# Performance work log

Measured on AMD Instinct MI355X. Metric: run time of the kernel, lower is better.

Reference implementation:

```python
import jax, jax.numpy as jnp
import numpy as np

N = 100000   # nodes
E = 1600000  # edges
IN, H, C = 128, 128, 40


def setup_inputs() -> dict:
    key = jax.random.key(0)
    ks = jax.random.split(key, 8)
    feat = jax.random.normal(ks[0], (N, IN), jnp.float32)
    src = jax.random.randint(ks[1], (E,), 0, N, jnp.int32)
    dst = jax.random.randint(ks[2], (E,), 0, N, jnp.int32)
    # Glorot-ish init like dgl GraphConv.reset_parameters
    W0 = jax.random.normal(ks[3], (IN, H), jnp.float32) * (1.0 / np.sqrt(IN))
    W1 = jax.random.normal(ks[4], (H, H), jnp.float32) * (1.0 / np.sqrt(H))
    W2 = jax.random.normal(ks[5], (H, C), jnp.float32) * (1.0 / np.sqrt(H))
    b0 = jnp.zeros((H,), jnp.float32)
    b1 = jnp.zeros((H,), jnp.float32)
    b2 = jnp.zeros((C,), jnp.float32)
    return {"feat": feat, "src": src, "dst": dst,
            "W0": W0, "b0": b0, "W1": W1, "b1": b1, "W2": W2, "b2": b2}


def _graph_conv(h, src, dst, W, b):
    # dgl GraphConv with norm='both': D_out^{-1/2} pre-scale, sum-aggregate,
    # D_in^{-1/2} post-scale; degrees clamped to min 1. Weight applied before
    # aggregation (in_feats >= out_feats path) -- math is identical either way.
    ones = jnp.ones((src.shape[0],), h.dtype)
    deg_out = jnp.maximum(jax.ops.segment_sum(ones, src, num_segments=N), 1.0)
    deg_in = jnp.maximum(jax.ops.segment_sum(ones, dst, num_segments=N), 1.0)
    h = h * (deg_out ** -0.5)[:, None]
    h = h @ W                                   # [N, out]
    agg = jax.ops.segment_sum(h[src], dst, num_segments=N)  # gather+scatter
    return agg * (deg_in ** -0.5)[:, None] + b


def reference(feat, src, dst, W0, b0, W1, b1, W2, b2):
    h = jax.nn.relu(_graph_conv(feat, src, dst, W0, b0))  # dropout p=0 -> identity
    h = jax.nn.relu(_graph_conv(h, src, dst, W1, b1))
    return _graph_conv(h, src, dst, W2, b2)
```

## Files before the change

kernel.cpp:

```cpp
#include <hip/hip_runtime.h>

#define NN 100000
#define EE 1600000
#define ELLW 64
#define GEMMN ((NN + 31) / 32)
#define BQ ((EE / 4 + 511) / 512)
#define GRID_BG (BQ * 5)

#define NBKT 196
#define BSH 9
#define CAPD 10240
#define CAPS 10240

typedef int iv4 __attribute__((ext_vector_type(4)));

__device__ __forceinline__ unsigned int pack_bf2(float a, float b) {
    unsigned int ua = __float_as_uint(a);
    ua += 0x7FFFu + ((ua >> 16) & 1u);
    unsigned int ub = __float_as_uint(b);
    ub += 0x7FFFu + ((ub >> 16) & 1u);
    return (ua >> 16) | (ub & 0xFFFF0000u);
}

__device__ __forceinline__ void gemm128_body(const float* __restrict__ X,
                                             const float* __restrict__ W, unsigned int* __restrict__ Y,
                                             int row0, int tid, float* Xs) {
    const float4* X4 = (const float4*)X;
#pragma unroll
    for (int idx = tid; idx < 1024; idx += 256) {
        int r = idx & 31, c4 = idx >> 5;
        int row = row0 + r;
        float4 v = X4[(size_t)row * 32 + c4];
        Xs[(c4 * 4 + 0) * 32 + r] = v.x;
        Xs[(c4 * 4 + 1) * 32 + r] = v.y;
        Xs[(c4 * 4 + 2) * 32 + r] = v.z;
        Xs[(c4 * 4 + 3) * 32 + r] = v.w;
    }
    __syncthreads();
    int cg = tid & 31;
    int rg = tid >> 5;
    float a[4][4];
#pragma unroll
    for (int r = 0; r < 4; ++r)
#pragma unroll
        for (int c = 0; c < 4; ++c) a[r][c] = 0.f;
    const float4* W4 = (const float4*)W;
#pragma unroll 4
    for (int k = 0; k < 128; ++k) {
        float4 xv = *(const float4*)&Xs[k * 32 + rg * 4];
        float4 wv = W4[k * 32 + cg];
        float xr[4] = {xv.x, xv.y, xv.z, xv.w};
        float wc[4] = {wv.x, wv.y, wv.z, wv.w};
#pragma unroll
        for (int r = 0; r < 4; ++r)
#pragma unroll
            for (int c = 0; c < 4; ++c) a[r][c] = fmaf(xr[r], wc[c], a[r][c]);
    }
    int rbase = row0 + rg * 4;
    uint2* Y2 = (uint2*)Y;
#pragma unroll
    for (int r = 0; r < 4; ++r) {
        Y2[(size_t)(rbase + r) * 32 + cg] =
            make_uint2(pack_bf2(a[r][0], a[r][1]), pack_bf2(a[r][2], a[r][3]));
    }
}

__global__ __launch_bounds__(256) void k_buildA_gemm0(const int* __restrict__ src, const int* __restrict__ dst,
                                                      int* __restrict__ curD, int* __restrict__ curS,
                                                      unsigned int* __restrict__ stagD,
                                                      unsigned short* __restrict__ stagS,
                                                      const float* __restrict__ X, const float* __restrict__ W,
                                                      unsigned int* __restrict__ Y) {
    __shared__ float Xs[128 * 32];
    int tid = threadIdx.x;
    int q = blockIdx.x / 5, rem = blockIdx.x % 5;
    if (rem) {
        int g = q * 4 + (rem - 1);
        if (g < GEMMN) gemm128_body(X, W, Y, g * 32, tid, Xs);
        return;
    }
    int* sh = (int*)Xs;
    for (int i = tid; i < 1536; i += 256) sh[i] = 0;
    __syncthreads();

    const iv4* s4p = (const iv4*)src;
    const iv4* d4p = (const iv4*)dst;
    const int n4 = EE / 4;
    iv4 sv[2], dv[2];
    int have[2];
#pragma unroll
    for (int h = 0; h < 2; ++h) {
        int i4 = q * 512 + h * 256 + tid;
        have[h] = (i4 < n4);
        if (have[h]) {
            sv[h] = __builtin_nontemporal_load(&s4p[i4]);
            dv[h] = __builtin_nontemporal_load(&d4p[i4]);
        }
    }
#pragma unroll
    for (int h = 0; h < 2; ++h) {
        if (have[h]) {
            int ss[4] = {sv[h].x, sv[h].y, sv[h].z, sv[h].w};
            int dd[4] = {dv[h].x, dv[h].y, dv[h].z, dv[h].w};
#pragma unroll
            for (int k = 0; k < 4; ++k) {
                atomicAdd(&sh[dd[k] >> BSH], 1);
                atomicAdd(&sh[256 + (ss[k] >> BSH)], 1);
            }
        }
    }
    __syncthreads();
    if (tid < NBKT) {
        int hd = sh[tid];
        sh[512 + tid] = hd ? atomicAdd(&curD[tid], hd) : 0;
        int hs = sh[256 + tid];
        sh[768 + tid] = hs ? atomicAdd(&curS[tid], hs) : 0;
    }
    __syncthreads();
#pragma unroll
    for (int h = 0; h < 2; ++h) {
        if (have[h]) {
            int ss[4] = {sv[h].x, sv[h].y, sv[h].z, sv[h].w};
            int dd[4] = {dv[h].x, dv[h].y, dv[h].z, dv[h].w};
#pragma unroll
            for (int k = 0; k < 4; ++k) {
                int bd = dd[k] >> BSH;
                int od = atomicAdd(&sh[1024 + bd], 1);
                stagD[(size_t)bd * CAPD + sh[512 + bd] + od] =
                    ((unsigned int)ss[k] << BSH) | (unsigned int)(dd[k] & 511);
                int bs = ss[k] >> BSH;
                int os = atomicAdd(&sh[1280 + bs], 1);
                stagS[(size_t)bs * CAPS + sh[768 + bs] + os] = (unsigned short)(ss[k] & 511);
            }
        }
    }
}

__global__ __launch_bounds__(256) void k_buildB(const int* __restrict__ curD, const int* __restrict__ curS,
                                                const unsigned int* __restrict__ stagD,
                                                const unsigned short* __restrict__ stagS,
                                                int* __restrict__ din, int* __restrict__ dout,
                                                int* __restrict__ ell) {
    __shared__ int cl[512];
    int tid = threadIdx.x;
    int b = blockIdx.x;
    for (int i = tid; i < 512; i += 256) cl[i] = 0;
    __syncthreads();
    if (b < NBKT) {
        int n0 = b << BSH;
        int cnt = min(curD[b], CAPD);
        const unsigned int* sg = stagD + (size_t)b * CAPD;
        for (int i = tid; i < cnt; i += 256) {
            unsigned int v = sg[i];
            int dlow = (int)(v & 511u);
            int s = (int)(v >> BSH);
            int p = atomicAdd(&cl[dlow], 1);
            if (p < ELLW) ell[(size_t)(n0 + dlow) * ELLW + p] = s;
        }
        __syncthreads();
        for (int i = tid; i < 512; i += 256) {
            int node = n0 + i;
            if (node < NN) din[node] = cl[i];
        }
    } else {
        int bs = b - NBKT;
        int n0 = bs << BSH;
        int cnt = min(curS[bs], CAPS);
        const unsigned short* sg = stagS + (size_t)bs * CAPS;
        for (int i = tid; i < cnt; i += 256) {
            atomicAdd(&cl[sg[i]], 1);
        }
        __syncthreads();
        for (int i = tid; i < 512; i += 256) {
            int node = n0 + i;
            if (node < NN) dout[node] = cl[i];
        }
    }
}

#define GG_BATCH(CL, SC, JB, CNT, SO) do {                                         \
    int cc_[8]; float mk_[8]; uint2 t_[8];                                         \
    _Pragma("unroll")                                                              \
    for (int k = 0; k < 8; ++k) {                                                  \
        int slot = (JB) + k;                                                       \
        int srcl = (hl << 5) | (slot & 31);                                        \
        cc_[k] = __shfl((CL), srcl);                                               \
        float sw = (SO) ? __shfl((SC), srcl) : 1.f;                                \
        mk_[k] = (slot < (CNT)) ? sw : 0.f;                                        \
    }                                                                              \
    _Pragma("unroll")                                                              \
    for (int k = 0; k < 8; ++k) {                                                  \
        t_[k] = make_uint2(0u, 0u);                                                \
        if ((JB) + k < (CNT)) t_[k] = h2v[(size_t)cc_[k] * 32 + ln];               \
    }                                                                              \
    _Pragma("unroll")                                                              \
    for (int k = 0; k < 8; ++k) {                                                  \
        a0 = fmaf(mk_[k], __uint_as_float(t_[k].x << 16), a0);                     \
        a1 = fmaf(mk_[k], __uint_as_float(t_[k].x & 0xFFFF0000u), a1);             \
        a2 = fmaf(mk_[k], __uint_as_float(t_[k].y << 16), a2);                     \
        a3 = fmaf(mk_[k], __uint_as_float(t_[k].y & 0xFFFF0000u), a3);             \
    }                                                                              \
} while (0)

__global__ __launch_bounds__(256) void k_gathergemm128(const unsigned int* __restrict__ h,
                                                       const int* __restrict__ din, const int* __restrict__ dout,
                                                       const int* __restrict__ ell,
                                                       const float* __restrict__ bias,
                                                       const float* __restrict__ W,
                                                       unsigned int* __restrict__ Y, int so_mode) {
    __shared__ float Xs[128 * 36];
    int tid = threadIdx.x;
    int wv = tid >> 6, lane = tid & 63;
    int hl = lane >> 5, ln = lane & 31;
    int row0 = blockIdx.x * 32;
    int nb = row0 + wv * 8 + hl;
    int dvh[4], dvo[4], cl0[4], cl1[4];
    float sc0[4], sc1[4];
#pragma unroll
    for (int it = 0; it < 4; ++it) {
        int v = nb + it * 2;
        dvh[it] = din[v];
        dvo[it] = dout[v];
        cl0[it] = ell[(size_t)v * ELLW + ln];
        cl1[it] = ell[(size_t)v * ELLW + 32 + ln];
    }
#pragma unroll
    for (int it = 0; it < 4; ++it) {
        int cnt = min(dvh[it], ELLW);
        int d0 = 1, d1 = 1;
        if (so_mode && ln < cnt) d0 = dout[cl0[it]];
        if (so_mode && ln + 32 < cnt) d1 = dout[cl1[it]];
        sc0[it] = rsqrtf((float)max(1, d0));
        sc1[it] = rsqrtf((float)max(1, d1));
    }
    float4 bb = ((const float4*)bias)[ln];
    const uint2* h2v = (const uint2*)h;
#pragma unroll
    for (int it = 0; it < 4; ++it) {
        int r = wv * 8 + it * 2 + hl;
        int cnt = min(dvh[it], ELLW);
        float a0 = 0.f, a1 = 0.f, a2 = 0.f, a3 = 0.f;
        for (int jb = 0; jb < 32; jb += 8) {
            if (!__any(jb < cnt)) break;
            GG_BATCH(cl0[it], sc0[it], jb, cnt, so_mode);
        }
        if (__any(cnt > 32)) {
            for (int jb = 32; jb < 64; jb += 8) {
                if (!__any(jb < cnt)) break;
                GG_BATCH(cl1[it], sc1[it], jb, cnt, so_mode);
            }
        }
        float si = rsqrtf((float)max(1, dvh[it]));
        float so = rsqrtf((float)max(1, dvo[it]));
        Xs[(4 * ln + 0) * 36 + r] = fmaxf(a0 * si + bb.x, 0.f) * so;
        Xs[(4 * ln + 1) * 36 + r] = fmaxf(a1 * si + bb.y, 0.f) * so;
        Xs[(4 * ln + 2) * 36 + r] = fmaxf(a2 * si + bb.z, 0.f) * so;
        Xs[(4 * ln + 3) * 36 + r] = fmaxf(a3 * si + bb.w, 0.f) * so;
    }
    __syncthreads();
    int cg = tid & 31, rg = tid >> 5;
    float a[4][4];
#pragma unroll
    for (int r = 0; r < 4; ++r)
#pragma unroll
        for (int c = 0; c < 4; ++c) a[r][c] = 0.f;
    const float4* W4 = (const float4*)W;
#pragma unroll 4
    for (int k = 0; k < 128; ++k) {
        float4 xv = *(const float4*)&Xs[k * 36 + rg * 4];
        float4 wv4 = W4[k * 32 + cg];
        float xr[4] = {xv.x, xv.y, xv.z, xv.w};
        float wc[4] = {wv4.x, wv4.y, wv4.z, wv4.w};
#pragma unroll
        for (int r = 0; r < 4; ++r)
#pragma unroll
            for (int c = 0; c < 4; ++c) a[r][c] = fmaf(xr[r], wc[c], a[r][c]);
    }
    int rbase = row0 + rg * 4;
    uint2* Y2 = (uint2*)Y;
#pragma unroll
    for (int r = 0; r < 4; ++r) {
        Y2[(size_t)(rbase + r) * 32 + cg] =
            make_uint2(pack_bf2(a[r][0], a[r][1]), pack_bf2(a[r][2], a[r][3]));
    }
}

__global__ __launch_bounds__(256) void k_gathergemm40(const unsigned int* __restrict__ h,
                                                      const int* __restrict__ din, const int* __restrict__ dout,
                                                      const int* __restrict__ ell,
                                                      const float* __restrict__ bias,
                                                      const float* __restrict__ W,
                                                      unsigned int* __restrict__ Y) {
    __shared__ float Xs[128 * 36];
    __shared__ float Os[32 * 40];
    int tid = threadIdx.x;
    int wv = tid >> 6, lane = tid & 63;
    int hl = lane >> 5, ln = lane & 31;
    int row0 = blockIdx.x * 32;
    int nb = row0 + wv * 8 + hl;
    int dvh[4], dvo[4], cl0[4], cl1[4];
#pragma unroll
    for (int it = 0; it < 4; ++it) {
        int v = nb + it * 2;
        dvh[it] = din[v];
        dvo[it] = dout[v];
        cl0[it] = ell[(size_t)v * ELLW + ln];
        cl1[it] = ell[(size_t)v * ELLW + 32 + ln];
    }
    float4 bb = ((const float4*)bias)[ln];
    const uint2* h2v = (const uint2*)h;
#pragma unroll
    for (int it = 0; it < 4; ++it) {
        int r = wv * 8 + it * 2 + hl;
        int cnt = min(dvh[it], ELLW);
        float a0 = 0.f, a1 = 0.f, a2 = 0.f, a3 = 0.f;
        float dummy = 0.f;
        for (int jb = 0; jb < 32; jb += 8) {
            if (!__any(jb < cnt)) break;
            GG_BATCH(cl0[it], dummy, jb, cnt, 0);
        }
        if (__any(cnt > 32)) {
            for (int jb = 32; jb < 64; jb += 8) {
                if (!__any(jb < cnt)) break;
                GG_BATCH(cl1[it], dummy, jb, cnt, 0);
            }
        }
        float si = rsqrtf((float)max(1, dvh[it]));
        float so = rsqrtf((float)max(1, dvo[it]));
        Xs[(4 * ln + 0) * 36 + r] = fmaxf(a0 * si + bb.x, 0.f) * so;
        Xs[(4 * ln + 1) * 36 + r] = fmaxf(a1 * si + bb.y, 0.f) * so;
        Xs[(4 * ln + 2) * 36 + r] = fmaxf(a2 * si + bb.z, 0.f) * so;
        Xs[(4 * ln + 3) * 36 + r] = fmaxf(a3 * si + bb.w, 0.f) * so;
    }
    __syncthreads();
    int rg = tid >> 3;
    int cg = tid & 7;
    float a[5] = {0.f, 0.f, 0.f, 0.f, 0.f};
    for (int k = 0; k < 128; ++k) {
        float x = Xs[k * 36 + rg];
#pragma unroll
        for (int c = 0; c < 5; ++c) a[c] = fmaf(x, W[k * 40 + cg * 5 + c], a[c]);
    }
#pragma unroll
    for (int c = 0; c < 5; ++c) Os[rg * 40 + cg * 5 + c] = a[c];
    __syncthreads();
    for (int i = tid; i < 640; i += 256) {
        int row = i / 20, pj = i % 20;
        Y[(size_t)(row0 + row) * 32 + pj] = pack_bf2(Os[row * 40 + 2 * pj], Os[row * 40 + 2 * pj + 1]);
    }
}

__global__ __launch_bounds__(256) void k_gather40(const unsigned int* __restrict__ h, const int* __restrict__ din,
                                                  const int* __restrict__ ell,
                                                  const float* __restrict__ b, float* __restrict__ out, int n) {
    int tid = threadIdx.x;
    int wv = tid >> 6, lane = tid & 63;
    int hl = lane >> 5, ln = lane & 31;
    int v = blockIdx.x * 8 + wv * 2 + hl;
    int dv = din[v];
    int cnt = min(dv, ELLW);
    int cl0 = ell[(size_t)v * ELLW + ln];
    int cl1 = ell[(size_t)v * ELLW + 32 + ln];
    float s0 = 0.f, s1 = 0.f;
    for (int half = 0; half < 2; ++half) {
        int clh = half ? cl1 : cl0;
        int jb0 = half * 32;
        if (half && !__any(cnt > 32)) break;
        for (int jb = jb0; jb < jb0 + 32; jb += 8) {
            if (!__any(jb < cnt)) break;
            int cc_[8]; float mk_[8]; unsigned int t_[8];
#pragma unroll
            for (int k = 0; k < 8; ++k) {
                int slot = jb + k;
                int srcl = (hl << 5) | (slot & 31);
                cc_[k] = __shfl(clh, srcl);
                mk_[k] = (slot < cnt) ? 1.f : 0.f;
            }
#pragma unroll
            for (int k = 0; k < 8; ++k) {
                t_[k] = 0u;
                if (jb + k < cnt) t_[k] = h[(size_t)cc_[k] * 32 + ln];
            }
#pragma unroll
            for (int k = 0; k < 8; ++k) {
                s0 = fmaf(mk_[k], __uint_as_float(t_[k] << 16), s0);
                s1 = fmaf(mk_[k], __uint_as_float(t_[k] & 0xFFFF0000u), s1);
            }
        }
    }
    if (ln < 20) {
        float si = rsqrtf((float)max(1, dv));
        float2 bb = ((const float2*)b)[ln];
        ((float2*)out)[(size_t)v * 20 + ln] = make_float2(s0 * si + bb.x, s1 * si + bb.y);
    }
}

extern "C" void kernel_launch(void* const* d_in, const int* in_sizes, int n_in,
                              void* d_out, int out_size, void* d_ws, size_t ws_size,
                              hipStream_t stream) {
    const float* feat = (const float*)d_in[0];
    const int*   src  = (const int*)d_in[1];
    const int*   dst  = (const int*)d_in[2];
    const float* W0   = (const float*)d_in[3];
    const float* b0   = (const float*)d_in[4];
    const float* W1   = (const float*)d_in[5];
    const float* b1   = (const float*)d_in[6];
    const float* W2   = (const float*)d_in[7];
    const float* b2   = (const float*)d_in[8];
    float* out = (float*)d_out;

    char* w = (char*)d_ws;
    int*   din       = (int*)w;    w += (size_t)NN * 4;
    int*   dout      = (int*)w;    w += (size_t)NN * 4;
    int*   curD      = (int*)w;    w += 256 * 4;
    int*   curS      = (int*)w;    w += 256 * 4;
    int*   ell       = (int*)w;    w += (size_t)NN * ELLW * 4;
    unsigned int*   stagD = (unsigned int*)w;   w += (size_t)NBKT * CAPD * 4;
    unsigned short* stagS = (unsigned short*)w; w += (size_t)NBKT * CAPS * 2;
    unsigned int* h2 = (unsigned int*)w; w += (size_t)NN * 128 * 2;
    unsigned int* h2b = (unsigned int*)w; w += (size_t)NN * 128 * 2;
    unsigned int* h40 = (unsigned int*)w; w += (size_t)NN * 32 * 4;

    (void)hipMemsetAsync(d_ws, 0, (size_t)NN * 8 + 2048, stream);

    k_buildA_gemm0<<<GRID_BG, 256, 0, stream>>>(src, dst, curD, curS, stagD, stagS, feat, W0, h2);
    k_buildB<<<NBKT * 2, 256, 0, stream>>>(curD, curS, stagD, stagS, din, dout, ell);
    k_gathergemm128<<<GEMMN, 256, 0, stream>>>(h2, din, dout, ell, b0, W1, h2b, 1);
    k_gathergemm40<<<GEMMN, 256, 0, stream>>>(h2b, din, dout, ell, b1, W2, h40);
    k_gather40<<<NN / 8, 256, 0, stream>>>(h40, din, ell, b2, out, NN);
}
```

Baseline: 480.0 us.

## Split fused gather+GEMM into half-width gather kernels and separate GEMM kernels

```diff
diff --git a/kernel.cpp b/kernel.cpp
--- a/kernel.cpp
+++ b/kernel.cpp
@@ -6,6 +6,7 @@
 #define GEMMN ((NN + 31) / 32)
 #define BQ ((EE / 4 + 511) / 512)
 #define GRID_BG (BQ * 5)
+#define GHGRID 6256
 
 #define NBKT 196
 #define BSH 9
@@ -178,41 +179,42 @@
     }
 }
 
-#define GG_BATCH(CL, SC, JB, CNT, SO) do {                                         \
-    int cc_[8]; float mk_[8]; uint2 t_[8];                                         \
+#define GH_BATCH(CL, SC, JB, CNT) do {                                             \
+    int cc_[8]; float mk_[8]; unsigned int t_[8];                                  \
     _Pragma("unroll")                                                              \
     for (int k = 0; k < 8; ++k) {                                                  \
         int slot = (JB) + k;                                                       \
         int srcl = (hl << 5) | (slot & 31);                                        \
         cc_[k] = __shfl((CL), srcl);                                               \
-        float sw = (SO) ? __shfl((SC), srcl) : 1.f;                                \
+        float sw = so_mode ? __shfl((SC), srcl) : 1.f;                             \
         mk_[k] = (slot < (CNT)) ? sw : 0.f;                                        \
     }                                                                              \
     _Pragma("unroll")                                                              \
     for (int k = 0; k < 8; ++k) {                                                  \
-        t_[k] = make_uint2(0u, 0u);                                                \
-        if ((JB) + k < (CNT)) t_[k] = h2v[(size_t)cc_[k] * 32 + ln];               \
+        t_[k] = 0u;                                                                \
+        if ((JB) + k < (CNT)) t_[k] = hh[(size_t)cc_[k] * 64 + ln];                \
     }                                                                              \
     _Pragma("unroll")                                                              \
     for (int k = 0; k < 8; ++k) {                                                  \
-        a0 = fmaf(mk_[k], __uint_as_float(t_[k].x << 16), a0);                     \
-        a1 = fmaf(mk_[k], __uint_as_float(t_[k].x & 0xFFFF0000u), a1);             \
-        a2 = fmaf(mk_[k], __uint_as_float(t_[k].y << 16), a2);                     \
-        a3 = fmaf(mk_[k], __uint_as_float(t_[k].y & 0xFFFF0000u), a3);             \
+        a0 = fmaf(mk_[k], __uint_as_float(t_[k] << 16), a0);                       \
+        a1 = fmaf(mk_[k], __uint_as_float(t_[k] & 0xFFFF0000u), a1);               \
     }                                                                              \
 } while (0)
 
-__global__ __launch_bounds__(256) void k_gathergemm128(const unsigned int* __restrict__ h,
-                                                       const int* __restrict__ din, const int* __restrict__ dout,
-                                                       const int* __restrict__ ell,
-                                                       const float* __restrict__ bias,
-                                                       const float* __restrict__ W,
-                                                       unsigned int* __restrict__ Y, int so_mode) {
-    __shared__ float Xs[128 * 36];
+__global__ __launch_bounds__(256) void k_gathalf(const unsigned int* __restrict__ h,
+                                                 const int* __restrict__ din, const int* __restrict__ dout,
+                                                 const int* __restrict__ ell,
+                                                 const float* __restrict__ bias,
+                                                 float* __restrict__ Xb, int so_mode) {
     int tid = threadIdx.x;
     int wv = tid >> 6, lane = tid & 63;
     int hl = lane >> 5, ln = lane & 31;
-    int row0 = blockIdx.x * 32;
+    int bid = blockIdx.x;
+    int xg = bid & 7;
+    int half = xg >> 2;
+    int t = (bid >> 3) * 4 + (xg & 3);
+    if (t >= GEMMN) return;
+    int row0 = t * 32;
     int nb = row0 + wv * 8 + hl;
     int dvh[4], dvo[4], cl0[4], cl1[4];
     float sc0[4], sc1[4];
@@ -233,111 +235,59 @@
         sc0[it] = rsqrtf((float)max(1, d0));
         sc1[it] = rsqrtf((float)max(1, d1));
     }
-    float4 bb = ((const float4*)bias)[ln];
-    const uint2* h2v = (const uint2*)h;
+    float2 bb = ((const float2*)bias)[32 * half + ln];
+    const unsigned int* hh = h + 32 * half;
 #pragma unroll
     for (int it = 0; it < 4; ++it) {
-        int r = wv * 8 + it * 2 + hl;
+        int v = nb + it * 2;
         int cnt = min(dvh[it], ELLW);
-        float a0 = 0.f, a1 = 0.f, a2 = 0.f, a3 = 0.f;
+        float a0 = 0.f, a1 = 0.f;
         for (int jb = 0; jb < 32; jb += 8) {
             if (!__any(jb < cnt)) break;
-            GG_BATCH(cl0[it], sc0[it], jb, cnt, so_mode);
+            GH_BATCH(cl0[it], sc0[it], jb, cnt);
         }
         if (__any(cnt > 32)) {
             for (int jb = 32; jb < 64; jb += 8) {
                 if (!__any(jb < cnt)) break;
-                GG_BATCH(cl1[it], sc1[it], jb, cnt, so_mode);
+                GH_BATCH(cl1[it], sc1[it], jb, cnt);
             }
         }
         float si = rsqrtf((float)max(1, dvh[it]));
         float so = rsqrtf((float)max(1, dvo[it]));
-        Xs[(4 * ln + 0) * 36 + r] = fmaxf(a0 * si + bb.x, 0.f) * so;
-        Xs[(4 * ln + 1) * 36 + r] = fmaxf(a1 * si + bb.y, 0.f) * so;
-        Xs[(4 * ln + 2) * 36 + r] = fmaxf(a2 * si + bb.z, 0.f) * so;
-        Xs[(4 * ln + 3) * 36 + r] = fmaxf(a3 * si + bb.w, 0.f) * so;
-    }
-    __syncthreads();
-    int cg = tid & 31, rg = tid >> 5;
-    float a[4][4];
-#pragma unroll
-    for (int r = 0; r < 4; ++r)
-#pragma unroll
-        for (int c = 0; c < 4; ++c) a[r][c] = 0.f;
-    const float4* W4 = (const float4*)W;
-#pragma unroll 4
-    for (int k = 0; k < 128; ++k) {
-        float4 xv = *(const float4*)&Xs[k * 36 + rg * 4];
-        float4 wv4 = W4[k * 32 + cg];
-        float xr[4] = {xv.x, xv.y, xv.z, xv.w};
-        float wc[4] = {wv4.x, wv4.y, wv4.z, wv4.w};
-#pragma unroll
-        for (int r = 0; r < 4; ++r)
-#pragma unroll
-            for (int c = 0; c < 4; ++c) a[r][c] = fmaf(xr[r], wc[c], a[r][c]);
-    }
-    int rbase = row0 + rg * 4;
-    uint2* Y2 = (uint2*)Y;
-#pragma unroll
-    for (int r = 0; r < 4; ++r) {
-        Y2[(size_t)(rbase + r) * 32 + cg] =
-            make_uint2(pack_bf2(a[r][0], a[r][1]), pack_bf2(a[r][2], a[r][3]));
-    }
-}
-
-__global__ __launch_bounds__(256) void k_gathergemm40(const unsigned int* __restrict__ h,
-                                                      const int* __restrict__ din, const int* __restrict__ dout,
-                                                      const int* __restrict__ ell,
-                                                      const float* __restrict__ bias,
-                                                      const float* __restrict__ W,
-                                                      unsigned int* __restrict__ Y) {
-    __shared__ float Xs[128 * 36];
+        float x0 = fmaxf(a0 * si + bb.x, 0.f) * so;
+        float x1 = fmaxf(a1 * si + bb.y, 0.f) * so;
+        ((float2*)Xb)[(size_t)v * 64 + 32 * half + ln] = make_float2(x0, x1);
+    }
+}
+
+__global__ __launch_bounds__(256) void k_gemm128(const float* __restrict__ X, const float* __restrict__ W,
+                                                 unsigned int* __restrict__ Y) {
+    __shared__ float Xs[128 * 32];
+    gemm128_body(X, W, Y, blockIdx.x * 32, threadIdx.x, Xs);
+}
+
+__global__ __launch_bounds__(256) void k_gemm40(const float* __restrict__ X, const float* __restrict__ W,
+                                                unsigned int* __restrict__ Y) {
+    __shared__ float Xs[128 * 32];
     __shared__ float Os[32 * 40];
     int tid = threadIdx.x;
-    int wv = tid >> 6, lane = tid & 63;
-    int hl = lane >> 5, ln = lane & 31;
     int row0 = blockIdx.x * 32;
-    int nb = row0 + wv * 8 + hl;
-    int dvh[4], dvo[4], cl0[4], cl1[4];
-#pragma unroll
-    for (int it = 0; it < 4; ++it) {
-        int v = nb + it * 2;
-        dvh[it] = din[v];
-        dvo[it] = dout[v];
-        cl0[it] = ell[(size_t)v * ELLW + ln];
-        cl1[it] = ell[(size_t)v * ELLW + 32 + ln];
-    }
-    float4 bb = ((const float4*)bias)[ln];
-    const uint2* h2v = (const uint2*)h;
-#pragma unroll
-    for (int it = 0; it < 4; ++it) {
-        int r = wv * 8 + it * 2 + hl;
-        int cnt = min(dvh[it], ELLW);
-        float a0 = 0.f, a1 = 0.f, a2 = 0.f, a3 = 0.f;
-        float dummy = 0.f;
-        for (int jb = 0; jb < 32; jb += 8) {
-            if (!__any(jb < cnt)) break;
-            GG_BATCH(cl0[it], dummy, jb, cnt, 0);
-        }
-        if (__any(cnt > 32)) {
-            for (int jb = 32; jb < 64; jb += 8) {
-                if (!__any(jb < cnt)) break;
-                GG_BATCH(cl1[it], dummy, jb, cnt, 0);
-            }
-        }
-        float si = rsqrtf((float)max(1, dvh[it]));
-        float so = rsqrtf((float)max(1, dvo[it]));
-        Xs[(4 * ln + 0) * 36 + r] = fmaxf(a0 * si + bb.x, 0.f) * so;
-        Xs[(4 * ln + 1) * 36 + r] = fmaxf(a1 * si + bb.y, 0.f) * so;
-        Xs[(4 * ln + 2) * 36 + r] = fmaxf(a2 * si + bb.z, 0.f) * so;
-        Xs[(4 * ln + 3) * 36 + r] = fmaxf(a3 * si + bb.w, 0.f) * so;
+    const float4* X4 = (const float4*)X;
+#pragma unroll
+    for (int idx = tid; idx < 1024; idx += 256) {
+        int r = idx & 31, c4 = idx >> 5;
+        float4 v = X4[(size_t)(row0 + r) * 32 + c4];
+        Xs[(c4 * 4 + 0) * 32 + r] = v.x;
+        Xs[(c4 * 4 + 1) * 32 + r] = v.y;
+        Xs[(c4 * 4 + 2) * 32 + r] = v.z;
+        Xs[(c4 * 4 + 3) * 32 + r] = v.w;
     }
     __syncthreads();
     int rg = tid >> 3;
     int cg = tid & 7;
     float a[5] = {0.f, 0.f, 0.f, 0.f, 0.f};
     for (int k = 0; k < 128; ++k) {
-        float x = Xs[k * 36 + rg];
+        float x = Xs[k * 32 + rg];
 #pragma unroll
         for (int c = 0; c < 5; ++c) a[c] = fmaf(x, W[k * 40 + cg * 5 + c], a[c]);
     }
@@ -415,17 +365,21 @@
     int*   curD      = (int*)w;    w += 256 * 4;
     int*   curS      = (int*)w;    w += 256 * 4;
     int*   ell       = (int*)w;    w += (size_t)NN * ELLW * 4;
-    unsigned int*   stagD = (unsigned int*)w;   w += (size_t)NBKT * CAPD * 4;
-    unsigned short* stagS = (unsigned short*)w; w += (size_t)NBKT * CAPS * 2;
     unsigned int* h2 = (unsigned int*)w; w += (size_t)NN * 128 * 2;
     unsigned int* h2b = (unsigned int*)w; w += (size_t)NN * 128 * 2;
     unsigned int* h40 = (unsigned int*)w; w += (size_t)NN * 32 * 4;
+    char* S = w;
+    unsigned int*   stagD = (unsigned int*)S;
+    unsigned short* stagS = (unsigned short*)(S + (size_t)NBKT * CAPD * 4);
+    float* Xb = (float*)S;
 
     (void)hipMemsetAsync(d_ws, 0, (size_t)NN * 8 + 2048, stream);
 
     k_buildA_gemm0<<<GRID_BG, 256, 0, stream>>>(src, dst, curD, curS, stagD, stagS, feat, W0, h2);
     k_buildB<<<NBKT * 2, 256, 0, stream>>>(curD, curS, stagD, stagS, din, dout, ell);
-    k_gathergemm128<<<GEMMN, 256, 0, stream>>>(h2, din, dout, ell, b0, W1, h2b, 1);
-    k_gathergemm40<<<GEMMN, 256, 0, stream>>>(h2b, din, dout, ell, b1, W2, h40);
+    k_gathalf<<<GHGRID, 256, 0, stream>>>(h2, din, dout, ell, b0, Xb, 1);
+    k_gemm128<<<GEMMN, 256, 0, stream>>>(Xb, W1, h2b);
+    k_gathalf<<<GHGRID, 256, 0, stream>>>(h2b, din, dout, ell, b1, Xb, 0);
+    k_gemm40<<<GEMMN, 256, 0, stream>>>(Xb, W2, h40);
     k_gather40<<<NN / 8, 256, 0, stream>>>(h40, din, ell, b2, out, NN);
 }
```

New measurement: 586.3 us. 22.1% more time.
